# Kernel tuning notes

Measured on AMD Instinct MI355X. Metric: run time of the kernel, lower is better.

The kernel has to match this reference:

```python
import jax, jax.numpy as jnp
import numpy as np

DIM = 768
HEADS = 12
HD = DIM // HEADS
SCALE = HD ** -0.5


def setup_inputs() -> dict:
    key = jax.random.key(0)
    ks = jax.random.split(key, 12)
    B, N = 2, 2048
    s = DIM ** -0.5
    return {
        "x1": jax.random.normal(ks[0], (B, N, DIM), jnp.float32),
        "x2": jax.random.normal(ks[1], (B, N, DIM), jnp.float32),
        "Wq": jax.random.normal(ks[2], (DIM, DIM), jnp.float32) * s,
        "bq": jax.random.normal(ks[3], (DIM,), jnp.float32) * 0.01,
        "Wk": jax.random.normal(ks[4], (DIM, DIM), jnp.float32) * s,
        "bk": jax.random.normal(ks[5], (DIM,), jnp.float32) * 0.01,
        "Wv": jax.random.normal(ks[6], (DIM, DIM), jnp.float32) * s,
        "bv": jax.random.normal(ks[7], (DIM,), jnp.float32) * 0.01,
        "Wo": jax.random.normal(ks[8], (DIM, DIM), jnp.float32) * s,
        "bo": jax.random.normal(ks[9], (DIM,), jnp.float32) * 0.01,
        "cross_scale": jnp.array([0.5], jnp.float32),
    }


def _heads(x, W, b):
    # torch Linear: x @ W.T + b; then (B,N,H,hd) -> (B,H,N,hd)
    B, N, _ = x.shape
    y = x @ W.T + b
    return y.reshape(B, N, HEADS, HD).transpose(0, 2, 1, 3)


def reference(x1, x2, Wq, bq, Wk, bk, Wv, bv, Wo, bo, cross_scale):
    B, N, C = x1.shape
    q1, k1, v1 = _heads(x1, Wq, bq), _heads(x1, Wk, bk), _heads(x1, Wv, bv)
    q2, k2, v2 = _heads(x2, Wq, bq), _heads(x2, Wk, bk), _heads(x2, Wv, bv)

    s = cross_scale[0]
    attn11 = jnp.einsum('bhqd,bhkd->bhqk', q1, k1) * SCALE
    attn22 = jnp.einsum('bhqd,bhkd->bhqk', q2, k2) * SCALE
    attn12 = jnp.einsum('bhqd,bhkd->bhqk', q1, k2) * SCALE
    attn21 = jnp.einsum('bhqd,bhkd->bhqk', q2, k1) * SCALE

    a1 = jax.nn.softmax((1.0 - s) * attn11 + s * attn12, axis=-1)
    a2 = jax.nn.softmax((1.0 - s) * attn22 + s * attn21, axis=-1)

    o1 = jnp.einsum('bhqk,bhkd->bhqd', a1, v1).transpose(0, 2, 1, 3).reshape(B, N, C)
    o2 = jnp.einsum('bhqk,bhkd->bhqd', a2, v2).transpose(0, 2, 1, 3).reshape(B, N, C)

    out1 = o1 @ Wo.T + bo
    out2 = o2 @ Wo.T + bo
    return out1, out2
```

## Files before the change

### kernel.cpp

```cpp
#include <hip/hip_runtime.h>

#define KDIM 768
#define HALF 3145728
#define XAELEMS 6291456
#define WELEMS 589824
#define QS 0.18033688f

typedef __attribute__((ext_vector_type(8))) short short8;
typedef __attribute__((ext_vector_type(4))) short short4_;
typedef __attribute__((ext_vector_type(4))) float float4_;
typedef __attribute__((ext_vector_type(2))) unsigned int uint2_;

__device__ __forceinline__ unsigned short f2bf(float f) {
  unsigned int u = __float_as_uint(f);
  u += 0x7fffu + ((u >> 16) & 1u);
  return (unsigned short)(u >> 16);
}

__device__ __forceinline__ unsigned int pack2bf(float a, float b) {
  unsigned int ua = __float_as_uint(a) + 0x8000u;
  unsigned int ub = __float_as_uint(b) + 0x8000u;
  return __builtin_amdgcn_perm(ub, ua, 0x07060302);
}

__device__ __forceinline__ void gll16(const void* g, void* l) {
  __builtin_amdgcn_global_load_lds(
      (const __attribute__((address_space(1))) unsigned int*)g,
      (__attribute__((address_space(3))) unsigned int*)l, 16, 0, 0);
}

__global__ void prep_x_kernel(const float* __restrict__ x1, const float* __restrict__ x2,
                              const float* __restrict__ cs,
                              unsigned short* __restrict__ xa, unsigned short* __restrict__ xb) {
  const int i = (blockIdx.x * 256 + threadIdx.x) * 4;
  const float s = cs[0], t_ = 1.0f - s;
  float4 a = *(const float4*)(x1 + i);
  float4 b = *(const float4*)(x2 + i);
  ushort4 ua = { f2bf(a.x), f2bf(a.y), f2bf(a.z), f2bf(a.w) };
  ushort4 ub = { f2bf(b.x), f2bf(b.y), f2bf(b.z), f2bf(b.w) };
  *(ushort4*)(xa + i) = ua;
  *(ushort4*)(xa + HALF + i) = ub;
  ushort4 c1 = { f2bf(t_*a.x + s*b.x), f2bf(t_*a.y + s*b.y), f2bf(t_*a.z + s*b.z), f2bf(t_*a.w + s*b.w) };
  ushort4 c2 = { f2bf(t_*b.x + s*a.x), f2bf(t_*b.y + s*a.y), f2bf(t_*b.z + s*a.z), f2bf(t_*b.w + s*a.w) };
  *(ushort4*)(xb + i) = c1;
  *(ushort4*)(xb + HALF + i) = c2;
}

__global__ void conv_w4_kernel(const float* __restrict__ w0, const float* __restrict__ w1,
                               const float* __restrict__ w2, const float* __restrict__ w3,
                               unsigned short* __restrict__ o0, unsigned short* __restrict__ o1,
                               unsigned short* __restrict__ o2, unsigned short* __restrict__ o3) {
  const int z = blockIdx.y;
  const float* w = (z == 0) ? w0 : (z == 1) ? w1 : (z == 2) ? w2 : w3;
  unsigned short* o = (z == 0) ? o0 : (z == 1) ? o1 : (z == 2) ? o2 : o3;
  const int i = (blockIdx.x * 256 + threadIdx.x) * 4;
  float4 a = *(const float4*)(w + i);
  ushort4 ua = { f2bf(a.x), f2bf(a.y), f2bf(a.z), f2bf(a.w) };
  *(ushort4*)(o + i) = ua;
}

__device__ __forceinline__ void gemm_mainloop(const unsigned short* __restrict__ A,
                                              const unsigned short* __restrict__ W,
                                              unsigned short* As, unsigned short* Bs,
                                              int m0, int n0, int t, float4_ (&acc)[4][4]) {
  const int lane = t & 63, quad = lane >> 4, lrow = lane & 15;
  const int wave = t >> 6;
  const int wm = (wave & 1) * 64, wn = (wave >> 1) * 64;
  for (int kt = 0; kt < KDIM; kt += 64) {
#pragma unroll
    for (int i = 0; i < 4; i++) {
      const int li = i * 256 + t;
      const int row = li >> 3, cc = (li & 7) * 8;
      gll16(A + (size_t)(m0 + row) * KDIM + kt + cc, As + li * 8);
      gll16(W + (size_t)(n0 + row) * KDIM + kt + cc, Bs + li * 8);
    }
    __syncthreads();
#pragma unroll
    for (int kk = 0; kk < 2; kk++) {
      short8 af[4], bfr[4];
#pragma unroll
      for (int i = 0; i < 4; i++)
        af[i] = *(const short8*)(As + (wm + i * 16 + lrow) * 64 + kk * 32 + quad * 8);
#pragma unroll
      for (int j = 0; j < 4; j++)
        bfr[j] = *(const short8*)(Bs + (wn + j * 16 + lrow) * 64 + kk * 32 + quad * 8);
#pragma unroll
      for (int i = 0; i < 4; i++)
#pragma unroll
        for (int j = 0; j < 4; j++)
          acc[i][j] = __builtin_amdgcn_mfma_f32_16x16x32_bf16(af[i], bfr[j], acc[i][j], 0, 0, 0);
    }
    __syncthreads();
  }
}

__global__ __launch_bounds__(256, 2)
void qkv_gemm(const unsigned short* __restrict__ xa, const unsigned short* __restrict__ xb,
              const unsigned short* __restrict__ wq, const unsigned short* __restrict__ wk,
              const unsigned short* __restrict__ wv,
              const float* __restrict__ bq, const float* __restrict__ bk, const float* __restrict__ bv,
              unsigned short* __restrict__ qo, unsigned short* __restrict__ ko,
              unsigned short* __restrict__ vto) {
  __shared__ __align__(16) unsigned short smem[16384];
  unsigned short* As = smem;
  unsigned short* Bs = smem + 8192;
  const int t = threadIdx.x;
  const int z = blockIdx.z;
  const int m0 = blockIdx.x * 128, n0 = blockIdx.y * 128;
  const unsigned short* A = (z == 1) ? xb : xa;
  const unsigned short* W = (z == 0) ? wq : (z == 1) ? wk : wv;
  const float* bias = (z == 0) ? bq : (z == 1) ? bk : bv;
  float4_ acc[4][4];
#pragma unroll
  for (int i = 0; i < 4; i++)
#pragma unroll
    for (int j = 0; j < 4; j++) acc[i][j] = (float4_){0.f, 0.f, 0.f, 0.f};
  gemm_mainloop(A, W, As, Bs, m0, n0, t, acc);

  const int lane = t & 63, quad = lane >> 4, lrow = lane & 15;
  const int wave = t >> 6;
  const int wm = (wave & 1) * 64, wn = (wave >> 1) * 64;

  if (z == 2) {
    unsigned short* Tb = smem + wave * 4096;
#pragma unroll
    for (int i = 0; i < 4; i++) {
#pragma unroll
      for (int j = 0; j < 4; j++) {
        const int nl = j * 16 + lrow;
        const float bn = bias[n0 + wn + nl];
#pragma unroll
        for (int r = 0; r < 4; r++) {
          const int ml = i * 16 + quad * 4 + r;
          const int c = ml >> 3;
          Tb[nl * 64 + ((c ^ (nl & 7)) * 8) + (ml & 7)] = f2bf(acc[i][j][r] + bn);
        }
      }
    }
    __asm__ __volatile__("s_waitcnt lgkmcnt(0)");
    const int sb = (m0 + wm) >> 11;
    const int hh = (n0 + wn) >> 6;
    const int tokbase = ((m0 + wm) & 2047);
#pragma unroll
    for (int i3 = 0; i3 < 8; i3++) {
      const int ci = i3 * 64 + lane;
      const int row = ci >> 3, p = ci & 7;
      short8 rd = *(const short8*)(Tb + row * 64 + p * 8);
      const int c = p ^ (row & 7);
      *(short8*)(vto + ((size_t)(sb * 12 + hh) * 64 + row) * 2048 + tokbase + c * 8) = rd;
    }
  } else {
    unsigned short* dst = (z == 0) ? qo : ko;
    const float scale = (z == 0) ? QS : 1.0f;
#pragma unroll
    for (int i = 0; i < 4; i++) {
#pragma unroll
      for (int j = 0; j < 4; j++) {
        const int n = n0 + wn + j * 16 + lrow;
        const float bn = bias[n];
#pragma unroll
        for (int r = 0; r < 4; r++) {
          const int m = m0 + wm + i * 16 + quad * 4 + r;
          dst[(size_t)m * KDIM + n] = f2bf((acc[i][j][r] + bn) * scale);
        }
      }
    }
  }
}

__global__ __launch_bounds__(256, 2)
void out_gemm(const unsigned short* __restrict__ ob, const unsigned short* __restrict__ wo,
              const float* __restrict__ bo, float* __restrict__ out) {
  __shared__ __align__(16) unsigned short As[128 * 64];
  __shared__ __align__(16) unsigned short Bs[128 * 64];
  const int t = threadIdx.x;
  const int m0 = blockIdx.x * 128, n0 = blockIdx.y * 128;
  float4_ acc[4][4];
#pragma unroll
  for (int i = 0; i < 4; i++)
#pragma unroll
    for (int j = 0; j < 4; j++) acc[i][j] = (float4_){0.f, 0.f, 0.f, 0.f};
  gemm_mainloop(ob, wo, As, Bs, m0, n0, t, acc);

  const int lane = t & 63, quad = lane >> 4, lrow = lane & 15;
  const int wave = t >> 6;
  const int wm = (wave & 1) * 64, wn = (wave >> 1) * 64;
#pragma unroll
  for (int i = 0; i < 4; i++) {
#pragma unroll
    for (int j = 0; j < 4; j++) {
      const int n = n0 + wn + j * 16 + lrow;
      const float bn = bo[n];
#pragma unroll
      for (int r = 0; r < 4; r++) {
        const int m = m0 + wm + i * 16 + quad * 4 + r;
        out[(size_t)m * KDIM + n] = acc[i][j][r] + bn;
      }
    }
  }
}

__global__ __launch_bounds__(256, 2)
void attn_kernel(const unsigned short* __restrict__ qg, const unsigned short* __restrict__ kg,
                 const unsigned short* __restrict__ vt, unsigned short* __restrict__ o) {
  __shared__ __align__(16) unsigned short Ks[2][64 * 64];
  __shared__ __align__(16) unsigned short Vs[2][64 * 64];
  const int prob = blockIdx.x % 48;
  const int q0 = (blockIdx.x / 48) * 128;
  const int sb = prob / 12, h = prob % 12;
  const int t = threadIdx.x, w = t >> 6, lane = t & 63, quad = lane >> 4, lrow = lane & 15;
  const int mbase = sb * 2048;
  const size_t vbase = (size_t)prob * (64 * 2048);

  short8 bq[2][2];
#pragma unroll
  for (int i = 0; i < 2; i++) {
    const unsigned short* qp = qg + (size_t)(mbase + q0 + w * 32 + i * 16 + lrow) * KDIM + h * 64 + quad * 8;
    bq[i][0] = *(const short8*)qp;
    bq[i][1] = *(const short8*)(qp + 32);
  }
  float l_part[2] = {0.f, 0.f};
  float4_ oa[2][4];
#pragma unroll
  for (int i = 0; i < 2; i++)
#pragma unroll
    for (int d = 0; d < 4; d++) oa[i][d] = (float4_){0.f, 0.f, 0.f, 0.f};

  auto stage = [&](int k0, int b) {
#pragma unroll
    for (int i2 = 0; i2 < 2; i2++) {
      const int li = i2 * 256 + t;
      const int row = li >> 3, p = li & 7;
      const int c = p ^ (row & 7);
      gll16(kg + (size_t)(mbase + k0 + row) * KDIM + h * 64 + c * 8, &Ks[b][li * 8]);
    }
#pragma unroll
    for (int i2 = 0; i2 < 2; i2++) {
      const int li = i2 * 256 + t;
      const int row = li >> 3, p = li & 7;
      const int c = p ^ (row & 7);
      gll16(vt + vbase + (size_t)row * 2048 + k0 + c * 8, &Vs[b][li * 8]);
    }
  };
  stage(0, 0);

  for (int kt = 0; kt < 32; kt++) {
    __syncthreads();
    const int b = kt & 1;
    if (kt + 1 < 32) stage((kt + 1) * 64, b ^ 1);

    float4_ st[4][2];
#pragma unroll
    for (int nt = 0; nt < 4; nt++)
#pragma unroll
      for (int i = 0; i < 2; i++) st[nt][i] = (float4_){0.f, 0.f, 0.f, 0.f};
    __builtin_amdgcn_s_setprio(1);
#pragma unroll
    for (int kk = 0; kk < 2; kk++) {
#pragma unroll
      for (int nt = 0; nt < 4; nt++) {
        short8 ak = *(const short8*)(&Ks[b][(nt * 16 + lrow) * 64 + (((kk * 4 + quad) ^ (lrow & 7)) * 8)]);
        st[nt][0] = __builtin_amdgcn_mfma_f32_16x16x32_bf16(ak, bq[0][kk], st[nt][0], 0, 0, 0);
        st[nt][1] = __builtin_amdgcn_mfma_f32_16x16x32_bf16(ak, bq[1][kk], st[nt][1], 0, 0, 0);
      }
    }
    __builtin_amdgcn_s_setprio(0);

    short4_ pb[2][4];
#pragma unroll
    for (int nt = 0; nt < 4; nt++)
#pragma unroll
      for (int i = 0; i < 2; i++) {
        const float p0 = __builtin_amdgcn_exp2f(st[nt][i][0]);
        const float p1 = __builtin_amdgcn_exp2f(st[nt][i][1]);
        const float p2 = __builtin_amdgcn_exp2f(st[nt][i][2]);
        const float p3 = __builtin_amdgcn_exp2f(st[nt][i][3]);
        l_part[i] += (p0 + p1) + (p2 + p3);
        uint2_ uu = { pack2bf(p0, p1), pack2bf(p2, p3) };
        pb[i][nt] = __builtin_bit_cast(short4_, uu);
      }

    __builtin_amdgcn_s_setprio(1);
#pragma unroll
    for (int g = 0; g < 2; g++) {
      const int cp0 = (((g * 4 + (quad >> 1)) ^ (lrow & 7)) * 8) + (quad & 1) * 4;
      const int cp1 = (((g * 4 + 2 + (quad >> 1)) ^ (lrow & 7)) * 8) + (quad & 1) * 4;
      const short8 b80 = __builtin_shufflevector(pb[0][2 * g], pb[0][2 * g + 1], 0, 1, 2, 3, 4, 5, 6, 7);
      const short8 b81 = __builtin_shufflevector(pb[1][2 * g], pb[1][2 * g + 1], 0, 1, 2, 3, 4, 5, 6, 7);
#pragma unroll
      for (int dt = 0; dt < 4; dt++) {
        const int rb = (dt * 16 + lrow) * 64;
        short4_ av0 = *(const short4_*)(&Vs[b][rb + cp0]);
        short4_ av1 = *(const short4_*)(&Vs[b][rb + cp1]);
        short8 a8 = __builtin_shufflevector(av0, av1, 0, 1, 2, 3, 4, 5, 6, 7);
        oa[0][dt] = __builtin_amdgcn_mfma_f32_16x16x32_bf16(a8, b80, oa[0][dt], 0, 0, 0);
        oa[1][dt] = __builtin_amdgcn_mfma_f32_16x16x32_bf16(a8, b81, oa[1][dt], 0, 0, 0);
      }
    }
    __builtin_amdgcn_s_setprio(0);
  }

#pragma unroll
  for (int i = 0; i < 2; i++) {
    float l = l_part[i];
    l += __shfl_xor(l, 16);
    l += __shfl_xor(l, 32);
    const float inv = 1.0f / l;
    const size_t m = (size_t)mbase + q0 + w * 32 + i * 16 + lrow;
#pragma unroll
    for (int dt = 0; dt < 4; dt++) {
      uint2_ uu = { pack2bf(oa[i][dt][0] * inv, oa[i][dt][1] * inv),
                    pack2bf(oa[i][dt][2] * inv, oa[i][dt][3] * inv) };
      *(uint2_*)(o + m * KDIM + h * 64 + dt * 16 + quad * 4) = uu;
    }
  }
}

extern "C" void kernel_launch(void* const* d_in, const int* in_sizes, int n_in,
                              void* d_out, int out_size, void* d_ws, size_t ws_size,
                              hipStream_t stream) {
  const float* x1 = (const float*)d_in[0];
  const float* x2 = (const float*)d_in[1];
  const float* Wq = (const float*)d_in[2];
  const float* bq = (const float*)d_in[3];
  const float* Wk = (const float*)d_in[4];
  const float* bk = (const float*)d_in[5];
  const float* Wv = (const float*)d_in[6];
  const float* bv = (const float*)d_in[7];
  const float* Wo = (const float*)d_in[8];
  const float* bo = (const float*)d_in[9];
  const float* cs = (const float*)d_in[10];
  float* out = (float*)d_out;

  char* ws = (char*)d_ws;
  size_t off = 0;
  auto alloc = [&](size_t bytes) {
    void* p = ws + off;
    off += (bytes + 255) & ~(size_t)255;
    return p;
  };
  unsigned short* xa  = (unsigned short*)alloc((size_t)XAELEMS * 2);
  unsigned short* xb  = (unsigned short*)alloc((size_t)XAELEMS * 2);
  unsigned short* wqb = (unsigned short*)alloc((size_t)WELEMS * 2);
  unsigned short* wkb = (unsigned short*)alloc((size_t)WELEMS * 2);
  unsigned short* wvb = (unsigned short*)alloc((size_t)WELEMS * 2);
  unsigned short* wob = (unsigned short*)alloc((size_t)WELEMS * 2);
  unsigned short* qg  = (unsigned short*)alloc((size_t)XAELEMS * 2);
  unsigned short* kgb = (unsigned short*)alloc((size_t)XAELEMS * 2);
  unsigned short* vtb = (unsigned short*)alloc((size_t)XAELEMS * 2);
  unsigned short* ob  = (unsigned short*)alloc((size_t)XAELEMS * 2);

  prep_x_kernel<<<HALF / 1024, 256, 0, stream>>>(x1, x2, cs, xa, xb);
  conv_w4_kernel<<<dim3(WELEMS / 1024, 4), 256, 0, stream>>>(Wq, Wk, Wv, Wo, wqb, wkb, wvb, wob);
  qkv_gemm<<<dim3(64, 6, 3), 256, 0, stream>>>(xa, xb, wqb, wkb, wvb, bq, bk, bv, qg, kgb, vtb);
  attn_kernel<<<48 * 16, 256, 0, stream>>>(qg, kgb, vtb, ob);
  out_gemm<<<dim3(64, 6), 256, 0, stream>>>(ob, wob, bo, out);
}
```

Measured before the change: 228.6 us.

## Triple-buffer K/V tiles in attention with explicit vmcnt waits and raw barriers

The attention kernel's K/V shared-memory staging moves from double to triple buffering. Each step issues loads two tiles ahead and waits with a partial vmcnt before a raw s_barrier, so one tile's loads can stay in flight while another is computed. The setprio hints around the MFMA blocks are removed. LDS use rises to 48KB per block, which may limit two-blocks-per-CU occupancy, and the hand-written vmcnt counts depend on each stage issuing exactly four loads.

```diff
diff --git a/kernel.cpp b/kernel.cpp
--- a/kernel.cpp
+++ b/kernel.cpp
@@ -203,8 +203,8 @@
 __global__ __launch_bounds__(256, 2)
 void attn_kernel(const unsigned short* __restrict__ qg, const unsigned short* __restrict__ kg,
                  const unsigned short* __restrict__ vt, unsigned short* __restrict__ o) {
-  __shared__ __align__(16) unsigned short Ks[2][64 * 64];
-  __shared__ __align__(16) unsigned short Vs[2][64 * 64];
+  __shared__ __align__(16) unsigned short Ks[3][64 * 64];
+  __shared__ __align__(16) unsigned short Vs[3][64 * 64];
   const int prob = blockIdx.x % 48;
   const int q0 = (blockIdx.x / 48) * 128;
   const int sb = prob / 12, h = prob % 12;
@@ -242,19 +242,13 @@
       gll16(vt + vbase + (size_t)row * 2048 + k0 + c * 8, &Vs[b][li * 8]);
     }
   };
-  stage(0, 0);
-
-  for (int kt = 0; kt < 32; kt++) {
-    __syncthreads();
-    const int b = kt & 1;
-    if (kt + 1 < 32) stage((kt + 1) * 64, b ^ 1);
-
+
+  auto compute = [&](int b) {
     float4_ st[4][2];
 #pragma unroll
     for (int nt = 0; nt < 4; nt++)
 #pragma unroll
       for (int i = 0; i < 2; i++) st[nt][i] = (float4_){0.f, 0.f, 0.f, 0.f};
-    __builtin_amdgcn_s_setprio(1);
 #pragma unroll
     for (int kk = 0; kk < 2; kk++) {
 #pragma unroll
@@ -264,7 +258,6 @@
         st[nt][1] = __builtin_amdgcn_mfma_f32_16x16x32_bf16(ak, bq[1][kk], st[nt][1], 0, 0, 0);
       }
     }
-    __builtin_amdgcn_s_setprio(0);
 
     short4_ pb[2][4];
 #pragma unroll
@@ -280,7 +273,6 @@
         pb[i][nt] = __builtin_bit_cast(short4_, uu);
       }
 
-    __builtin_amdgcn_s_setprio(1);
 #pragma unroll
     for (int g = 0; g < 2; g++) {
       const int cp0 = (((g * 4 + (quad >> 1)) ^ (lrow & 7)) * 8) + (quad & 1) * 4;
@@ -297,8 +289,34 @@
         oa[1][dt] = __builtin_amdgcn_mfma_f32_16x16x32_bf16(a8, b81, oa[1][dt], 0, 0, 0);
       }
     }
-    __builtin_amdgcn_s_setprio(0);
-  }
+  };
+
+  stage(0, 0);
+  stage(64, 1);
+
+#define STEP(KT, CUR, STG)                                   \
+  do {                                                       \
+    asm volatile("s_waitcnt vmcnt(4)" ::: "memory");         \
+    __builtin_amdgcn_s_barrier();                            \
+    __builtin_amdgcn_sched_barrier(0);                       \
+    stage(((KT) + 2) * 64, (STG));                           \
+    compute(CUR);                                            \
+  } while (0)
+
+  for (int kt0 = 0; kt0 < 30; kt0 += 3) {
+    STEP(kt0, 0, 2);
+    STEP(kt0 + 1, 1, 0);
+    STEP(kt0 + 2, 2, 1);
+  }
+  asm volatile("s_waitcnt vmcnt(4)" ::: "memory");
+  __builtin_amdgcn_s_barrier();
+  __builtin_amdgcn_sched_barrier(0);
+  compute(0);
+  asm volatile("s_waitcnt vmcnt(0)" ::: "memory");
+  __builtin_amdgcn_s_barrier();
+  __builtin_amdgcn_sched_barrier(0);
+  compute(1);
+#undef STEP
 
 #pragma unroll
   for (int i = 0; i < 2; i++) {
```

After: 224.2 us. About the same (-1.9%).
